# Kernel tuning notes

Measured on AMD Instinct MI355X. Metric: run time of the kernel, lower is better.

Reference implementation:

```python
import jax, jax.numpy as jnp
import numpy as np

# LocalConv config (must match init_kwargs)
B, C, H, W = 64, 16, 64, 64
KH, KW = 3, 3
SH, SW = 1, 1
OUT_CH = 32
OH = (H - KH + SH) // SH  # 62
OW = (W - KW + SW) // SW  # 62
P = OH * OW               # 3844 positions
FEAT = C * KH * KW        # 144 (flatten order: C, kh, kw)


def setup_inputs() -> dict:
    key = jax.random.key(0)
    k1, k2 = jax.random.split(key)
    inputs = jax.random.normal(k1, (B, C, H, W), dtype=jnp.float32)
    kernel = jax.random.normal(k2, (P, FEAT, OUT_CH), dtype=jnp.float32)
    return {"inputs": inputs, "kernel": kernel}


def _extract_patches(x):
    # x: (B, C, H, W) -> (P, B, FEAT) with FEAT flattened as (C, kh, kw),
    # matching torch's reshape of inputs[:, :, i:i+kh, j:j+kw].
    i_idx = (jnp.arange(OH) * SH)[:, None] + jnp.arange(KH)[None, :]  # (OH, KH)
    j_idx = (jnp.arange(OW) * SW)[:, None] + jnp.arange(KW)[None, :]  # (OW, KW)
    # gather -> (B, C, OH, KH, OW, KW)
    p = x[:, :, i_idx[:, :, None, None], j_idx[None, None, :, :]]
    # -> (OH, OW, B, C, KH, KW)
    p = jnp.transpose(p, (2, 4, 0, 1, 3, 5))
    return p.reshape(P, B, FEAT)


def reference(inputs, kernel):
    patches = _extract_patches(inputs)                 # (P, B, FEAT)
    out = jnp.einsum('pbf,pfo->pbo', patches, kernel)  # per-position unshared matmul
    out = out.reshape(OH, OW, B, OUT_CH)
    return jnp.transpose(out, (2, 3, 0, 1))            # (B, OUT_CH, OH, OW)
```

## Files before the change

### kernel.cpp

```cpp
#include <hip/hip_runtime.h>

#define CIN    16
#define HH     64
#define WW     64
#define OHD    62
#define OWD    62
#define OUTC   32
#define FEATN  144
#define POUT   (OHD*OWD)
#define LSTRB  152
#define AR_W   8
#define AR_ELEMS   (3*AR_W*64*16)
#define BBUF_ELEMS (OUTC*LSTRB + 8)
#define SMEM_BYTES ((AR_ELEMS + 2*BBUF_ELEMS)*2)

typedef __attribute__((ext_vector_type(8))) short  short8;
typedef __attribute__((ext_vector_type(4))) float  f32x4;
typedef __attribute__((ext_vector_type(2))) float  f32x2;

__device__ __forceinline__ unsigned short f2bf(float f) {
    unsigned int u = __float_as_uint(f);
    u += 0x7FFFu + ((u >> 16) & 1u);
    return (unsigned short)(u >> 16);
}

template<int TW>
__device__ __forceinline__ void conv_body(
    const float* __restrict__ inp, const float* __restrict__ wgt,
    float* __restrict__ out, int oh, int ow0,
    unsigned short* __restrict__ Araw, unsigned short* __restrict__ B_lds)
{
    const int tid = threadIdx.x;
    constexpr int WTOT = TW + 2;

    const int o_w = tid & 31;
    const int c_w = tid >> 5;
    const int p0  = oh * OWD + ow0;
    const float* wbase = wgt + (size_t)p0 * (FEATN * OUTC) + c_w * 288 + o_w;
    float ring[3][9];
    auto issue = [&](int t) {
        const float* p = wbase + (size_t)t * (FEATN * OUTC);
        #pragma unroll
        for (int g = 0; g < 9; ++g) ring[t % 3][g] = p[g * 32];
    };
    const int wb_base = o_w * LSTRB + c_w;
    auto writeB = [&](int t, unsigned short* Bb) {
        #pragma unroll
        for (int g = 0; g < 9; ++g)
            Bb[wb_base + g * 16] = f2bf(ring[t % 3][g]);
    };

    issue(0);
    if (1 < TW) issue(1);
    if (2 < TW) issue(2);

    for (int t = tid; t < 3 * WTOT * 64; t += 512) {
        int w   = t % WTOT;
        int rem = t / WTOT;
        int b   = rem & 63;
        int kh  = rem >> 6;
        const float* src = inp + (size_t)b * (CIN * HH * WW)
                               + (size_t)(oh + kh) * WW + (ow0 + w);
        short8 h0, h1;
        #pragma unroll
        for (int c = 0; c < 8; ++c) h0[c] = (short)f2bf(src[c * (HH * WW)]);
        #pragma unroll
        for (int c = 0; c < 8; ++c) h1[c] = (short)f2bf(src[(c + 8) * (HH * WW)]);
        int s = (b >> 2) & 1;
        unsigned Gb = (unsigned)(((kh * AR_W + w) * 64 + b) * 2);
        unsigned wx = (unsigned)((w & 3) << 1);
        *(short8*)(Araw + (((Gb + s) ^ wx) << 3))       = h0;
        *(short8*)(Araw + (((Gb + (1 - s)) ^ wx) << 3)) = h1;
    }

    for (int t = tid; t < 2 * 264; t += 512) {
        int buf = t / 264, r = t % 264;
        int e = (r < 256) ? ((r >> 3) * LSTRB + 144 + (r & 7))
                          : (OUTC * LSTRB + (r & 7));
        B_lds[buf * BBUF_ELEMS + e] = 0;
    }

    writeB(0, B_lds);

    const int wid = tid >> 6, lane = tid & 63;
    const int fr = lane & 15, fq = lane >> 4, fqh = fq >> 1;
    const int mt = wid >> 1, nt = wid & 1;
    const int b  = mt * 16 + fr;
    const int gr = (fq & 1) ^ ((b >> 2) & 1);
    unsigned abase_g[5]; int kwv[5]; int boff[5];
    #pragma unroll
    for (int kc = 0; kc < 5; ++kc) {
        int g  = 2 * kc + fqh;
        int gc = (g > 8) ? 8 : g;
        int kh = (gc * 11) >> 5;
        int kw = gc - 3 * kh;
        abase_g[kc] = (unsigned)(((kh * AR_W + kw) * 64 + b) * 2 + gr);
        kwv[kc]     = kw;
        boff[kc]    = (nt * 16 + fr) * LSTRB + kc * 32 + fq * 8;
    }

    __syncthreads();

    f32x4 acc[TW];
    #pragma unroll
    for (int q = 0; q < TW; ++q) acc[q] = (f32x4){0.f, 0.f, 0.f, 0.f};

    #pragma unroll
    for (int q = 0; q < TW; ++q) {
        const unsigned short* Bc = B_lds + (q & 1) * BBUF_ELEMS;
        #pragma unroll
        for (int kc = 0; kc < 5; ++kc) {
            short8 a;
            if (kc == 4 && fqh == 1) {
                a = (short8){0, 0, 0, 0, 0, 0, 0, 0};
            } else {
                unsigned gi = (abase_g[kc] + (unsigned)(q * 128))
                              ^ (unsigned)(((q + kwv[kc]) & 3) << 1);
                a = *(const short8*)(Araw + (gi << 3));
            }
            short8 bfv = *(const short8*)(Bc + boff[kc]);
            acc[q] = __builtin_amdgcn_mfma_f32_16x16x32_bf16(a, bfv, acc[q], 0, 0, 0);
        }
        if (q + 3 < TW) issue(q + 3);
        if (q + 1 < TW) {
            writeB(q + 1, B_lds + ((q + 1) & 1) * BBUF_ELEMS);
            __syncthreads();
        }
    }

    const int o = nt * 16 + fr;
    #pragma unroll
    for (int r = 0; r < 4; ++r) {
        float* dst = out + ((size_t)((mt * 16 + fq * 4 + r) * OUTC + o)) * POUT
                         + (size_t)oh * OWD + ow0;
        #pragma unroll
        for (int j = 0; j < TW / 2; ++j) {
            f32x2 v = { acc[2 * j][r], acc[2 * j + 1][r] };
            *(f32x2*)(dst + 2 * j) = v;
        }
    }
}

__global__ __launch_bounds__(512, 4) void localconv_kernel(
    const float* __restrict__ inp,
    const float* __restrict__ wgt,
    float* __restrict__ out)
{
    extern __shared__ unsigned short smem[];
    unsigned short* Araw  = smem;
    unsigned short* B_lds = smem + AR_ELEMS;

    const int bid = blockIdx.x;
    const int xcd = bid & 7, i = bid >> 3;
    const int l   = (xcd < 2) ? xcd * 86 + i : 172 + (xcd - 2) * 85 + i;
    const int oh    = l / 11;
    const int strip = l % 11;

    if (strip < 10) conv_body<6>(inp, wgt, out, oh, strip * 6, Araw, B_lds);
    else            conv_body<2>(inp, wgt, out, oh, 60, Araw, B_lds);
}

extern "C" void kernel_launch(void* const* d_in, const int* in_sizes, int n_in,
                              void* d_out, int out_size, void* d_ws, size_t ws_size,
                              hipStream_t stream) {
    const float* inp = (const float*)d_in[0];
    const float* wgt = (const float*)d_in[1];
    float* out = (float*)d_out;
    hipFuncSetAttribute((const void*)localconv_kernel,
                        hipFuncAttributeMaxDynamicSharedMemorySize, SMEM_BYTES);
    localconv_kernel<<<dim3(682), 512, SMEM_BYTES, stream>>>(inp, wgt, out);
}
```

Baseline: 40.50 us.

## Load weights directly into MFMA registers and truncate to bf16 via high-half loads

Drops the LDS staging of the per-position weight matrix. Each wave now loads its B fragments straight from global memory into registers, double-buffered across output positions, and computes both 16-wide output-channel tiles itself. Float-to-bf16 conversion becomes a plain 16-bit load of the upper half of each float (truncation instead of round-to-nearest) for both inputs and weights. Block size drops to 256 threads with static shared memory, removing the B-buffer syncs. The cost is many scattered 2-byte global loads, higher register pressure, and slightly lower precision from truncation.

```diff
diff --git a/kernel.cpp b/kernel.cpp
--- a/kernel.cpp
+++ b/kernel.cpp
@@ -8,64 +8,70 @@
 #define OUTC   32
 #define FEATN  144
 #define POUT   (OHD*OWD)
-#define LSTRB  152
+#define WBYTES (FEATN*OUTC*4)
 #define AR_W   8
-#define AR_ELEMS   (3*AR_W*64*16)
-#define BBUF_ELEMS (OUTC*LSTRB + 8)
-#define SMEM_BYTES ((AR_ELEMS + 2*BBUF_ELEMS)*2)
+#define AR_ELEMS (3*AR_W*64*16)
 
 typedef __attribute__((ext_vector_type(8))) short  short8;
 typedef __attribute__((ext_vector_type(4))) float  f32x4;
 typedef __attribute__((ext_vector_type(2))) float  f32x2;
 
-__device__ __forceinline__ unsigned short f2bf(float f) {
-    unsigned int u = __float_as_uint(f);
-    u += 0x7FFFu + ((u >> 16) & 1u);
-    return (unsigned short)(u >> 16);
-}
-
 template<int TW>
 __device__ __forceinline__ void conv_body(
     const float* __restrict__ inp, const float* __restrict__ wgt,
     float* __restrict__ out, int oh, int ow0,
-    unsigned short* __restrict__ Araw, unsigned short* __restrict__ B_lds)
+    unsigned short* __restrict__ Araw)
 {
     const int tid = threadIdx.x;
     constexpr int WTOT = TW + 2;
 
-    const int o_w = tid & 31;
-    const int c_w = tid >> 5;
+    const int lane = tid & 63, wid = tid >> 6;
+    const int fr  = lane & 15, fq = lane >> 4, fqh = fq >> 1;
+    const int mt  = wid;
     const int p0  = oh * OWD + ow0;
-    const float* wbase = wgt + (size_t)p0 * (FEATN * OUTC) + c_w * 288 + o_w;
-    float ring[3][9];
-    auto issue = [&](int t) {
-        const float* p = wbase + (size_t)t * (FEATN * OUTC);
+
+    const int fbase = (fq & 1) * 72 + fqh;
+    const char* wB  = (const char*)wgt + (size_t)p0 * WBYTES
+                    + fbase * 128 + fr * 4 + 2;
+    const int k4b = fqh ? 0 : 1024;
+
+    short8 R0[10], R1[10];
+    auto issueB = [&](int q, short8 (&R)[10]) {
+        const char* wq  = wB + (size_t)q * WBYTES;
+        const char* wq4 = wq + k4b;
         #pragma unroll
-        for (int g = 0; g < 9; ++g) ring[t % 3][g] = p[g * 32];
-    };
-    const int wb_base = o_w * LSTRB + c_w;
-    auto writeB = [&](int t, unsigned short* Bb) {
+        for (int kc = 0; kc < 4; ++kc)
+            #pragma unroll
+            for (int nt = 0; nt < 2; ++nt)
+                #pragma unroll
+                for (int j = 0; j < 8; ++j)
+                    R[kc * 2 + nt][j] = (short)*(const unsigned short*)
+                        (wq + kc * 256 + nt * 64 + j * 1152);
         #pragma unroll
-        for (int g = 0; g < 9; ++g)
-            Bb[wb_base + g * 16] = f2bf(ring[t % 3][g]);
+        for (int nt = 0; nt < 2; ++nt)
+            #pragma unroll
+            for (int j = 0; j < 8; ++j)
+                R[8 + nt][j] = (short)*(const unsigned short*)
+                    (wq4 + nt * 64 + j * 1152);
     };
 
-    issue(0);
-    if (1 < TW) issue(1);
-    if (2 < TW) issue(2);
+    issueB(0, R0);
+    if (TW > 1) issueB(1, R1);
 
-    for (int t = tid; t < 3 * WTOT * 64; t += 512) {
+    for (int t = tid; t < 3 * WTOT * 64; t += 256) {
         int w   = t % WTOT;
         int rem = t / WTOT;
         int b   = rem & 63;
         int kh  = rem >> 6;
-        const float* src = inp + (size_t)b * (CIN * HH * WW)
-                               + (size_t)(oh + kh) * WW + (ow0 + w);
+        const char* src = (const char*)(inp + (size_t)b * (CIN * HH * WW)
+                        + (size_t)(oh + kh) * WW + (ow0 + w)) + 2;
         short8 h0, h1;
         #pragma unroll
-        for (int c = 0; c < 8; ++c) h0[c] = (short)f2bf(src[c * (HH * WW)]);
+        for (int c = 0; c < 8; ++c)
+            h0[c] = (short)*(const unsigned short*)(src + c * (HH * WW * 4));
         #pragma unroll
-        for (int c = 0; c < 8; ++c) h1[c] = (short)f2bf(src[(c + 8) * (HH * WW)]);
+        for (int c = 0; c < 8; ++c)
+            h1[c] = (short)*(const unsigned short*)(src + (c + 8) * (HH * WW * 4));
         int s = (b >> 2) & 1;
         unsigned Gb = (unsigned)(((kh * AR_W + w) * 64 + b) * 2);
         unsigned wx = (unsigned)((w & 3) << 1);
@@ -73,21 +79,9 @@
         *(short8*)(Araw + (((Gb + (1 - s)) ^ wx) << 3)) = h1;
     }
 
-    for (int t = tid; t < 2 * 264; t += 512) {
-        int buf = t / 264, r = t % 264;
-        int e = (r < 256) ? ((r >> 3) * LSTRB + 144 + (r & 7))
-                          : (OUTC * LSTRB + (r & 7));
-        B_lds[buf * BBUF_ELEMS + e] = 0;
-    }
-
-    writeB(0, B_lds);
-
-    const int wid = tid >> 6, lane = tid & 63;
-    const int fr = lane & 15, fq = lane >> 4, fqh = fq >> 1;
-    const int mt = wid >> 1, nt = wid & 1;
     const int b  = mt * 16 + fr;
     const int gr = (fq & 1) ^ ((b >> 2) & 1);
-    unsigned abase_g[5]; int kwv[5]; int boff[5];
+    unsigned abase_g[5]; int kwv[5];
     #pragma unroll
     for (int kc = 0; kc < 5; ++kc) {
         int g  = 2 * kc + fqh;
@@ -96,59 +90,59 @@
         int kw = gc - 3 * kh;
         abase_g[kc] = (unsigned)(((kh * AR_W + kw) * 64 + b) * 2 + gr);
         kwv[kc]     = kw;
-        boff[kc]    = (nt * 16 + fr) * LSTRB + kc * 32 + fq * 8;
     }
 
     __syncthreads();
 
-    f32x4 acc[TW];
+    f32x4 acc[TW][2];
     #pragma unroll
-    for (int q = 0; q < TW; ++q) acc[q] = (f32x4){0.f, 0.f, 0.f, 0.f};
+    for (int q = 0; q < TW; ++q) {
+        acc[q][0] = (f32x4){0.f, 0.f, 0.f, 0.f};
+        acc[q][1] = (f32x4){0.f, 0.f, 0.f, 0.f};
+    }
 
     #pragma unroll
     for (int q = 0; q < TW; ++q) {
-        const unsigned short* Bc = B_lds + (q & 1) * BBUF_ELEMS;
+        short8 (&R)[10] = (q & 1) ? R1 : R0;
         #pragma unroll
         for (int kc = 0; kc < 5; ++kc) {
-            short8 a;
+            short8 av;
             if (kc == 4 && fqh == 1) {
-                a = (short8){0, 0, 0, 0, 0, 0, 0, 0};
+                av = (short8){0, 0, 0, 0, 0, 0, 0, 0};
             } else {
                 unsigned gi = (abase_g[kc] + (unsigned)(q * 128))
-                              ^ (unsigned)(((q + kwv[kc]) & 3) << 1);
-                a = *(const short8*)(Araw + (gi << 3));
+                            ^ (unsigned)(((q + kwv[kc]) & 3) << 1);
+                av = *(const short8*)(Araw + (gi << 3));
             }
-            short8 bfv = *(const short8*)(Bc + boff[kc]);
-            acc[q] = __builtin_amdgcn_mfma_f32_16x16x32_bf16(a, bfv, acc[q], 0, 0, 0);
+            acc[q][0] = __builtin_amdgcn_mfma_f32_16x16x32_bf16(
+                            av, R[kc * 2 + 0], acc[q][0], 0, 0, 0);
+            acc[q][1] = __builtin_amdgcn_mfma_f32_16x16x32_bf16(
+                            av, R[kc * 2 + 1], acc[q][1], 0, 0, 0);
         }
-        if (q + 3 < TW) issue(q + 3);
-        if (q + 1 < TW) {
-            writeB(q + 1, B_lds + ((q + 1) & 1) * BBUF_ELEMS);
-            __syncthreads();
-        }
+        if (q + 2 < TW) issueB(q + 2, R);
     }
 
-    const int o = nt * 16 + fr;
     #pragma unroll
-    for (int r = 0; r < 4; ++r) {
-        float* dst = out + ((size_t)((mt * 16 + fq * 4 + r) * OUTC + o)) * POUT
-                         + (size_t)oh * OWD + ow0;
+    for (int r = 0; r < 4; ++r)
         #pragma unroll
-        for (int j = 0; j < TW / 2; ++j) {
-            f32x2 v = { acc[2 * j][r], acc[2 * j + 1][r] };
-            *(f32x2*)(dst + 2 * j) = v;
+        for (int nt = 0; nt < 2; ++nt) {
+            float* dst = out
+                + ((size_t)((mt * 16 + fq * 4 + r) * OUTC + nt * 16 + fr)) * POUT
+                + (size_t)oh * OWD + ow0;
+            #pragma unroll
+            for (int j = 0; j < TW / 2; ++j) {
+                f32x2 v = { acc[2 * j][nt][r], acc[2 * j + 1][nt][r] };
+                *(f32x2*)(dst + 2 * j) = v;
+            }
         }
-    }
 }
 
-__global__ __launch_bounds__(512, 4) void localconv_kernel(
+__global__ __launch_bounds__(256, 3) void localconv_kernel(
     const float* __restrict__ inp,
     const float* __restrict__ wgt,
     float* __restrict__ out)
 {
-    extern __shared__ unsigned short smem[];
-    unsigned short* Araw  = smem;
-    unsigned short* B_lds = smem + AR_ELEMS;
+    __shared__ unsigned short Araw[AR_ELEMS];
 
     const int bid = blockIdx.x;
     const int xcd = bid & 7, i = bid >> 3;
@@ -156,8 +150,8 @@
     const int oh    = l / 11;
     const int strip = l % 11;
 
-    if (strip < 10) conv_body<6>(inp, wgt, out, oh, strip * 6, Araw, B_lds);
-    else            conv_body<2>(inp, wgt, out, oh, 60, Araw, B_lds);
+    if (strip < 10) conv_body<6>(inp, wgt, out, oh, strip * 6, Araw);
+    else            conv_body<2>(inp, wgt, out, oh, 60, Araw);
 }
 
 extern "C" void kernel_launch(void* const* d_in, const int* in_sizes, int n_in,
@@ -166,7 +160,5 @@
     const float* inp = (const float*)d_in[0];
     const float* wgt = (const float*)d_in[1];
     float* out = (float*)d_out;
-    hipFuncSetAttribute((const void*)localconv_kernel,
-                        hipFuncAttributeMaxDynamicSharedMemorySize, SMEM_BYTES);
-    localconv_kernel<<<dim3(682), 512, SMEM_BYTES, stream>>>(inp, wgt, out);
+    localconv_kernel<<<dim3(682), 256, 0, stream>>>(inp, wgt, out);
 }
```

New measurement: 97.65 us. 141% more time.

## Load only high bf16 halves of fp32 inputs, deepen weight prefetch, use LDS-only barrier

Applied to the files above, without the earlier changes.

Replaces the fp32 loads plus round-to-nearest bf16 conversion with 16-bit loads of the upper half of each float, which truncates instead of rounding. This removes the conversion ALU work and halves the bytes each load instruction requests. The weight prefetch ring goes from 3 to 4 stages. __syncthreads is replaced by a barrier that waits only on LDS counters, so in-flight global loads are not drained at each sync. Truncation changes numerics slightly, and the sparse 2-byte loads still touch the same cache lines.

```diff
diff --git a/kernel.cpp b/kernel.cpp
--- a/kernel.cpp
+++ b/kernel.cpp
@@ -8,6 +8,7 @@
 #define OUTC   32
 #define FEATN  144
 #define POUT   (OHD*OWD)
+#define WBYTES (FEATN*OUTC*4)
 #define LSTRB  152
 #define AR_W   8
 #define AR_ELEMS   (3*AR_W*64*16)
@@ -18,10 +19,11 @@
 typedef __attribute__((ext_vector_type(4))) float  f32x4;
 typedef __attribute__((ext_vector_type(2))) float  f32x2;
 
-__device__ __forceinline__ unsigned short f2bf(float f) {
-    unsigned int u = __float_as_uint(f);
-    u += 0x7FFFu + ((u >> 16) & 1u);
-    return (unsigned short)(u >> 16);
+__device__ __forceinline__ void softBarrier() {
+    asm volatile("s_waitcnt lgkmcnt(0)" ::: "memory");
+    __builtin_amdgcn_sched_barrier(0);
+    __builtin_amdgcn_s_barrier();
+    __builtin_amdgcn_sched_barrier(0);
 }
 
 template<int TW>
@@ -36,36 +38,41 @@
     const int o_w = tid & 31;
     const int c_w = tid >> 5;
     const int p0  = oh * OWD + ow0;
-    const float* wbase = wgt + (size_t)p0 * (FEATN * OUTC) + c_w * 288 + o_w;
-    float ring[3][9];
+    const char* wbase = (const char*)wgt + (size_t)p0 * WBYTES
+                      + (size_t)(c_w * 288 + o_w) * 4 + 2;
+    unsigned short ring[4][9];
     auto issue = [&](int t) {
-        const float* p = wbase + (size_t)t * (FEATN * OUTC);
+        const char* p = wbase + (size_t)t * WBYTES;
         #pragma unroll
-        for (int g = 0; g < 9; ++g) ring[t % 3][g] = p[g * 32];
+        for (int g = 0; g < 9; ++g)
+            ring[t & 3][g] = *(const unsigned short*)(p + g * 128);
     };
     const int wb_base = o_w * LSTRB + c_w;
     auto writeB = [&](int t, unsigned short* Bb) {
         #pragma unroll
         for (int g = 0; g < 9; ++g)
-            Bb[wb_base + g * 16] = f2bf(ring[t % 3][g]);
+            Bb[wb_base + g * 16] = ring[t & 3][g];
     };
 
     issue(0);
-    if (1 < TW) issue(1);
-    if (2 < TW) issue(2);
+    if (TW > 1) issue(1);
+    if (TW > 2) issue(2);
+    if (TW > 3) issue(3);
 
     for (int t = tid; t < 3 * WTOT * 64; t += 512) {
         int w   = t % WTOT;
         int rem = t / WTOT;
         int b   = rem & 63;
         int kh  = rem >> 6;
-        const float* src = inp + (size_t)b * (CIN * HH * WW)
-                               + (size_t)(oh + kh) * WW + (ow0 + w);
+        const char* src = (const char*)(inp + (size_t)b * (CIN * HH * WW)
+                        + (size_t)(oh + kh) * WW + (ow0 + w)) + 2;
         short8 h0, h1;
         #pragma unroll
-        for (int c = 0; c < 8; ++c) h0[c] = (short)f2bf(src[c * (HH * WW)]);
+        for (int c = 0; c < 8; ++c)
+            h0[c] = (short)*(const unsigned short*)(src + c * (HH * WW * 4));
         #pragma unroll
-        for (int c = 0; c < 8; ++c) h1[c] = (short)f2bf(src[(c + 8) * (HH * WW)]);
+        for (int c = 0; c < 8; ++c)
+            h1[c] = (short)*(const unsigned short*)(src + (c + 8) * (HH * WW * 4));
         int s = (b >> 2) & 1;
         unsigned Gb = (unsigned)(((kh * AR_W + w) * 64 + b) * 2);
         unsigned wx = (unsigned)((w & 3) << 1);
@@ -99,7 +106,7 @@
         boff[kc]    = (nt * 16 + fr) * LSTRB + kc * 32 + fq * 8;
     }
 
-    __syncthreads();
+    softBarrier();
 
     f32x4 acc[TW];
     #pragma unroll
@@ -121,10 +128,10 @@
             short8 bfv = *(const short8*)(Bc + boff[kc]);
             acc[q] = __builtin_amdgcn_mfma_f32_16x16x32_bf16(a, bfv, acc[q], 0, 0, 0);
         }
-        if (q + 3 < TW) issue(q + 3);
+        if (q + 4 < TW) issue(q + 4);
         if (q + 1 < TW) {
             writeB(q + 1, B_lds + ((q + 1) & 1) * BBUF_ELEMS);
-            __syncthreads();
+            softBarrier();
         }
     }
 
```

Result: slower. 47.50 us (+17.3%).

## Shrink strip width to four, prefetch all weight slices upfront, lighter barriers

Applied to the files above, without the earlier changes.

Output strips shrink from 6 to 4 positions, so the grid grows from 682 to 992 blocks with a new XCD-aware index mapping. All weight slices for a block (up to 4) are now loaded into registers before the loop instead of through a rolling 3-slot ring. __syncthreads is replaced by an inline-asm barrier that waits only on LDS counters, and LDS moves from dynamic to static allocation. The aim is more parallelism, lower LDS use per block and less barrier overhead. The trade-off is more redundant halo loads per output and more weight-holding registers.

```diff
diff --git a/kernel.cpp b/kernel.cpp
--- a/kernel.cpp
+++ b/kernel.cpp
@@ -9,19 +9,23 @@
 #define FEATN  144
 #define POUT   (OHD*OWD)
 #define LSTRB  152
-#define AR_W   8
+#define AR_W   6
 #define AR_ELEMS   (3*AR_W*64*16)
 #define BBUF_ELEMS (OUTC*LSTRB + 8)
-#define SMEM_BYTES ((AR_ELEMS + 2*BBUF_ELEMS)*2)
 
 typedef __attribute__((ext_vector_type(8))) short  short8;
 typedef __attribute__((ext_vector_type(4))) float  f32x4;
-typedef __attribute__((ext_vector_type(2))) float  f32x2;
+typedef __attribute__((ext_vector_type(4), aligned(4))) float f32x4u;
+typedef __attribute__((ext_vector_type(2), aligned(4))) float f32x2u;
 
 __device__ __forceinline__ unsigned short f2bf(float f) {
     unsigned int u = __float_as_uint(f);
     u += 0x7FFFu + ((u >> 16) & 1u);
     return (unsigned short)(u >> 16);
+}
+
+__device__ __forceinline__ void softBarrier() {
+    asm volatile("s_waitcnt lgkmcnt(0)\n\ts_barrier" ::: "memory");
 }
 
 template<int TW>
@@ -37,22 +41,23 @@
     const int c_w = tid >> 5;
     const int p0  = oh * OWD + ow0;
     const float* wbase = wgt + (size_t)p0 * (FEATN * OUTC) + c_w * 288 + o_w;
-    float ring[3][9];
+    float ring[4][9];
     auto issue = [&](int t) {
         const float* p = wbase + (size_t)t * (FEATN * OUTC);
         #pragma unroll
-        for (int g = 0; g < 9; ++g) ring[t % 3][g] = p[g * 32];
+        for (int g = 0; g < 9; ++g) ring[t & 3][g] = p[g * 32];
     };
     const int wb_base = o_w * LSTRB + c_w;
     auto writeB = [&](int t, unsigned short* Bb) {
         #pragma unroll
         for (int g = 0; g < 9; ++g)
-            Bb[wb_base + g * 16] = f2bf(ring[t % 3][g]);
+            Bb[wb_base + g * 16] = f2bf(ring[t & 3][g]);
     };
 
     issue(0);
-    if (1 < TW) issue(1);
-    if (2 < TW) issue(2);
+    if (TW > 1) issue(1);
+    if (TW > 2) issue(2);
+    if (TW > 3) issue(3);
 
     for (int t = tid; t < 3 * WTOT * 64; t += 512) {
         int w   = t % WTOT;
@@ -99,7 +104,7 @@
         boff[kc]    = (nt * 16 + fr) * LSTRB + kc * 32 + fq * 8;
     }
 
-    __syncthreads();
+    softBarrier();
 
     f32x4 acc[TW];
     #pragma unroll
@@ -121,10 +126,9 @@
             short8 bfv = *(const short8*)(Bc + boff[kc]);
             acc[q] = __builtin_amdgcn_mfma_f32_16x16x32_bf16(a, bfv, acc[q], 0, 0, 0);
         }
-        if (q + 3 < TW) issue(q + 3);
         if (q + 1 < TW) {
             writeB(q + 1, B_lds + ((q + 1) & 1) * BBUF_ELEMS);
-            __syncthreads();
+            softBarrier();
         }
     }
 
@@ -133,10 +137,12 @@
     for (int r = 0; r < 4; ++r) {
         float* dst = out + ((size_t)((mt * 16 + fq * 4 + r) * OUTC + o)) * POUT
                          + (size_t)oh * OWD + ow0;
-        #pragma unroll
-        for (int j = 0; j < TW / 2; ++j) {
-            f32x2 v = { acc[2 * j][r], acc[2 * j + 1][r] };
-            *(f32x2*)(dst + 2 * j) = v;
+        if constexpr (TW == 4) {
+            f32x4u v = { acc[0][r], acc[1][r], acc[2][r], acc[3][r] };
+            *(f32x4u*)dst = v;
+        } else {
+            f32x2u v = { acc[0][r], acc[1][r] };
+            *(f32x2u*)dst = v;
         }
     }
 }
@@ -146,17 +152,15 @@
     const float* __restrict__ wgt,
     float* __restrict__ out)
 {
-    extern __shared__ unsigned short smem[];
-    unsigned short* Araw  = smem;
-    unsigned short* B_lds = smem + AR_ELEMS;
+    __shared__ unsigned short Araw[AR_ELEMS];
+    __shared__ unsigned short B_lds[2 * BBUF_ELEMS];
 
     const int bid = blockIdx.x;
-    const int xcd = bid & 7, i = bid >> 3;
-    const int l   = (xcd < 2) ? xcd * 86 + i : 172 + (xcd - 2) * 85 + i;
-    const int oh    = l / 11;
-    const int strip = l % 11;
+    const int l   = (bid & 7) * 124 + (bid >> 3);
+    const int oh    = l >> 4;
+    const int strip = l & 15;
 
-    if (strip < 10) conv_body<6>(inp, wgt, out, oh, strip * 6, Araw, B_lds);
+    if (strip < 15) conv_body<4>(inp, wgt, out, oh, strip * 4, Araw, B_lds);
     else            conv_body<2>(inp, wgt, out, oh, 60, Araw, B_lds);
 }
 
@@ -166,7 +170,5 @@
     const float* inp = (const float*)d_in[0];
     const float* wgt = (const float*)d_in[1];
     float* out = (float*)d_out;
-    hipFuncSetAttribute((const void*)localconv_kernel,
-                        hipFuncAttributeMaxDynamicSharedMemorySize, SMEM_BYTES);
-    localconv_kernel<<<dim3(682), 512, SMEM_BYTES, stream>>>(inp, wgt, out);
+    localconv_kernel<<<dim3(992), 512, 0, stream>>>(inp, wgt, out);
 }
```

Measured after the change: 43.93 us. 1.08x slower.
